# Performance work log

Measured on AMD Instinct MI355X. Metric: run time of the kernel, lower is better.

## Reference

```python
import jax, jax.numpy as jnp
import numpy as np

B, N, D = 64, 128, 32
P = N * (N - 1)          # ordered pairs
H1, H2, HF = 32, 32, 16  # layer_widths=(32,32), final_widths=(16,)
EPS = 1e-5
SLOPE = 0.01             # LeakyReLU default


def _leaky(x):
    return jnp.where(x >= 0, x, SLOPE * x)


def setup_inputs() -> dict:
    key = jax.random.key(0)
    ks = jax.random.split(key, 16)
    # all ordered pairs (i, j), i != j, grouped by source i
    src = np.repeat(np.arange(N), N - 1)
    tgt = np.array([j for i in range(N) for j in range(N) if j != i])
    s = 0.1
    return {
        "inputs": jax.random.normal(ks[0], (B, N, D), jnp.float32),
        "src": jnp.asarray(src, jnp.int32),
        "tgt": jnp.asarray(tgt, jnp.int32),
        # edge MLP: Linear(2D,32) -> BN1d(P) -> LeakyReLU -> Linear(32,32) -> LeakyReLU -> Linear(32, 1+D)
        "W1": jax.random.normal(ks[1], (2 * D, H1), jnp.float32) * s,
        "b1": jnp.zeros((H1,), jnp.float32),
        "g1": jnp.ones((P,), jnp.float32),
        "be1": jnp.zeros((P,), jnp.float32),
        "W2": jax.random.normal(ks[2], (H1, H2), jnp.float32) * s,
        "b2": jnp.zeros((H2,), jnp.float32),
        "W3": jax.random.normal(ks[3], (H2, 1 + D), jnp.float32) * s,
        "b3": jnp.zeros((1 + D,), jnp.float32),
        # final MLP: Linear(2D,16) -> BN1d(16) -> LeakyReLU -> Linear(16, D)
        "Wf1": jax.random.normal(ks[4], (2 * D, HF), jnp.float32) * s,
        "bf1": jnp.zeros((HF,), jnp.float32),
        "gf": jnp.ones((HF,), jnp.float32),
        "bef": jnp.zeros((HF,), jnp.float32),
        "Wf2": jax.random.normal(ks[5], (HF, D), jnp.float32) * s,
        "bf2": jnp.zeros((D,), jnp.float32),
    }


def reference(inputs, src, tgt, W1, b1, g1, be1, W2, b2, W3, b3,
              Wf1, bf1, gf, bef, Wf2, bf2):
    b, n, d = inputs.shape
    # gather pair features: (B, P, 2D)
    paired = jnp.concatenate([inputs[:, src], inputs[:, tgt]], axis=2)
    h = paired @ W1 + b1                              # (B, P, H1)
    # BatchNorm1d(P) on (B, P, H1): normalize per pair channel over (batch, feat)
    m = h.mean(axis=(0, 2), keepdims=True)
    v = h.var(axis=(0, 2), keepdims=True)
    h = (h - m) * jax.lax.rsqrt(v + EPS) * g1[None, :, None] + be1[None, :, None]
    h = _leaky(h) @ W2 + b2
    h = _leaky(h) @ W3 + b3                           # (B, P, 1+D)
    edges = jax.nn.sigmoid(h[..., :1])                # (B, P, 1)
    messages = h[..., 1:]                             # (B, P, D)
    weighted = edges * messages
    # segment-sum over the (N-1) senders per source node
    agg = weighted.reshape(b, n, n - 1, d).sum(axis=2)  # (B, N, D)
    sm = jnp.concatenate([inputs, agg], axis=2).reshape(-1, 2 * d)
    f = sm @ Wf1 + bf1                                # (B*N, HF)
    mf = f.mean(axis=0)
    vf = f.var(axis=0)
    f = (f - mf) * jax.lax.rsqrt(vf + EPS) * gf + bef
    out = _leaky(f) @ Wf2 + bf2
    return edges[..., 0], out.reshape(b, n, d)
```

## Files before the change

### kernel.cpp

```cpp
#include <hip/hip_runtime.h>
#include <hip/hip_bf16.h>
#include <math.h>

#define BB 64
#define NN 128
#define DD 32
#define PP (NN * (NN - 1))
#define EPSF 1e-5f

typedef __attribute__((ext_vector_type(8))) short bf16x8;
typedef __attribute__((ext_vector_type(4))) float f32x4;

static __device__ __forceinline__ unsigned short f2bf(float x) {
    unsigned u = __builtin_bit_cast(unsigned, x);
    u += 0x7fff + ((u >> 16) & 1);
    return (unsigned short)(u >> 16);
}
static __device__ __forceinline__ unsigned pk2bf(float a, float b) {
    float2 t; t.x = a; t.y = b;
    __hip_bfloat162 h = __float22bfloat162_rn(t);
    unsigned u;
    __builtin_memcpy(&u, &h, 4);
    return u;
}
static __device__ __forceinline__ float leakyf(float x) {
    return fmaxf(x, 0.01f * x);
}

__global__ __launch_bounds__(256) void proj_kernel(
    const float* __restrict__ inputs, const float* __restrict__ W1,
    const float* __restrict__ b1,
    const float* __restrict__ W2, const float* __restrict__ W3,
    float* __restrict__ AT, float* __restrict__ BT,
    unsigned short* __restrict__ ATh, unsigned short* __restrict__ BTh,
    float* __restrict__ SQp,
    unsigned short* __restrict__ W2p, unsigned short* __restrict__ W3p,
    float* __restrict__ fpartA, float* __restrict__ fpartB)
{
    __shared__ float Xs[16 * 33];
    __shared__ float W1s[2048];
    __shared__ float red[16];

    int tid = threadIdx.x;
    int n = blockIdx.x >> 2, q = blockIdx.x & 3;

    for (int idx = tid; idx < 2048; idx += 256) W1s[idx] = W1[idx];
    for (int idx = tid; idx < 512; idx += 256) {
        int r = idx >> 5, d = idx & 31;
        Xs[r * 33 + d] = inputs[(size_t)(q * 16 + r) * 4096 + n * 32 + d];
    }
    __syncthreads();

    int j = tid & 31, rb = tid >> 5;
    int lane = tid & 63, w = tid >> 6;
    float b1j = b1[j];
    float sa = 0.f, qa = 0.f, sb = 0.f, qb = 0.f;
    #pragma unroll
    for (int i = 0; i < 2; ++i) {
        int r = rb * 2 + i;
        int b = q * 16 + r;
        float a = b1j, c = 0.f;
        #pragma unroll
        for (int k = 0; k < 32; ++k) {
            float x = Xs[r * 33 + k];
            a += x * W1s[k * 32 + j];
            c += x * W1s[(32 + k) * 32 + j];
        }
        size_t off = ((size_t)n * 64 + b) * 32 + j;
        AT[off] = a;  BT[off] = c;
        ATh[off] = f2bf(a);  BTh[off] = f2bf(c);
        sa += a; qa += a * a; sb += c; qb += c * c;
    }
    #pragma unroll
    for (int d = 32; d > 0; d >>= 1) {
        sa += __shfl_down(sa, d, 64);
        qa += __shfl_down(qa, d, 64);
        sb += __shfl_down(sb, d, 64);
        qb += __shfl_down(qb, d, 64);
    }
    if (lane == 0) { red[w*4+0] = sa; red[w*4+1] = qa; red[w*4+2] = sb; red[w*4+3] = qb; }
    __syncthreads();
    if (tid == 0) {
        float4 v;
        v.x = red[0] + red[4] + red[8]  + red[12];
        v.y = red[1] + red[5] + red[9]  + red[13];
        v.z = red[2] + red[6] + red[10] + red[14];
        v.w = red[3] + red[7] + red[11] + red[15];
        ((float4*)SQp)[n * 4 + q] = v;
    }

    if (blockIdx.x == 0 && tid < 64) {
        int l = tid, nn2 = l & 15, kc = l >> 4;
        #pragma unroll
        for (int ct = 0; ct < 2; ++ct)
            #pragma unroll
            for (int jj = 0; jj < 8; ++jj) {
                int k = kc * 8 + jj;
                W2p[(ct * 64 + l) * 8 + jj] = f2bf(W2[k * 32 + ct * 16 + nn2]);
            }
        #pragma unroll
        for (int ct = 0; ct < 3; ++ct)
            #pragma unroll
            for (int jj = 0; jj < 8; ++jj) {
                int k = kc * 8 + jj;
                int c2 = ct * 16 + nn2;
                W3p[(ct * 64 + l) * 8 + jj] = f2bf(c2 < 33 ? W3[k * 33 + c2] : 0.f);
            }
    }
    if (blockIdx.x == 1) {
        for (int idx = tid; idx < 1024; idx += 256) {
            fpartA[idx] = 0.f;
            fpartB[idx] = 0.f;
        }
    }
}

__global__ __launch_bounds__(256) void stats2_kernel(
    const unsigned short* __restrict__ ATh, const unsigned short* __restrict__ BTh,
    const float* __restrict__ SQp,
    const float* __restrict__ g1, const float* __restrict__ be1,
    float* __restrict__ statA, float* __restrict__ statB)
{
    __shared__ __align__(16) float part[4 * 64 * 4];
    int tid = threadIdx.x;
    int lane = tid & 63, w = tid >> 6;
    int s0 = (blockIdx.x >> 3) * 16, t0 = (blockIdx.x & 7) * 16;

    int m = lane & 15, kc = lane >> 4;
    const unsigned short* abase = ATh + (size_t)(s0 + m) * 2048 + kc * 8 + w * 512;
    const unsigned short* bbase = BTh + (size_t)(t0 + m) * 2048 + kc * 8 + w * 512;

    f32x4 acc0 = {0.f, 0.f, 0.f, 0.f}, acc1 = {0.f, 0.f, 0.f, 0.f};
    #pragma unroll
    for (int step = 0; step < 8; ++step) {
        bf16x8 av0 = *(const bf16x8*)(abase + (2 * step) * 32);
        bf16x8 bv0 = *(const bf16x8*)(bbase + (2 * step) * 32);
        acc0 = __builtin_amdgcn_mfma_f32_16x16x32_bf16(av0, bv0, acc0, 0, 0, 0);
        bf16x8 av1 = *(const bf16x8*)(abase + (2 * step + 1) * 32);
        bf16x8 bv1 = *(const bf16x8*)(bbase + (2 * step + 1) * 32);
        acc1 = __builtin_amdgcn_mfma_f32_16x16x32_bf16(av1, bv1, acc1, 0, 0, 0);
    }
    f32x4 acc;
    acc[0] = acc0[0] + acc1[0]; acc[1] = acc0[1] + acc1[1];
    acc[2] = acc0[2] + acc1[2]; acc[3] = acc0[3] + acc1[3];
    *(f32x4*)&part[(w * 64 + lane) * 4] = acc;
    __syncthreads();

    if (w == 0) {
        #pragma unroll
        for (int ww = 1; ww < 4; ++ww) {
            f32x4 o2 = *(const f32x4*)&part[(ww * 64 + lane) * 4];
            acc[0] += o2[0]; acc[1] += o2[1]; acc[2] += o2[2]; acc[3] += o2[3];
        }
        int col = lane & 15, quad = lane >> 4;
        int t = t0 + col;
        float sbt = 0.f, qbt = 0.f;
        #pragma unroll
        for (int o2 = 0; o2 < 4; ++o2) {
            float4 v = ((const float4*)SQp)[t * 4 + o2];
            sbt += v.z; qbt += v.w;
        }
        #pragma unroll
        for (int r = 0; r < 4; ++r) {
            int s = s0 + quad * 4 + r;
            if (s != t) {
                float sas = 0.f, qas = 0.f;
                #pragma unroll
                for (int o2 = 0; o2 < 4; ++o2) {
                    float4 v = ((const float4*)SQp)[s * 4 + o2];
                    sas += v.x; qas += v.y;
                }
                int e = t - (t > s);
                int p = s * 127 + e;
                float S = sas + sbt;
                float Q = qas + qbt + 2.f * acc[r];
                float mean = S * (1.f / 2048.f);
                float var  = Q * (1.f / 2048.f) - mean * mean;
                float inv  = rsqrtf(var + EPSF);
                float sc   = inv * g1[p];
                statA[p] = sc;
                statB[p] = be1[p] - mean * sc;
            }
        }
    }
}

__global__ __launch_bounds__(256) void edges_kernel(
    const float* __restrict__ AT, const float* __restrict__ BT,
    const float* __restrict__ statA, const float* __restrict__ statB,
    const unsigned short* __restrict__ W2p, const unsigned short* __restrict__ W3p,
    const float* __restrict__ b2, const float* __restrict__ b3,
    const float* __restrict__ inputs, const float* __restrict__ Wf1,
    const float* __restrict__ bf1,
    float* __restrict__ edges_out,
    float* __restrict__ f, float* __restrict__ fpartA, float* __restrict__ fpartB)
{
    __shared__ __align__(16) unsigned short Hs[4][512];
    __shared__ float Wf1s[1024];
    __shared__ float aggbuf[4][32];

    int tid = threadIdx.x;
    int s = blockIdx.x & 127;
    int b = blockIdx.x >> 7;
    int lane = tid & 63, w = tid >> 6;
    int m = lane & 15;
    int kb = lane >> 4;
    int col = m;
    int q4 = kb * 4;
    int qbase = lane & 48;

    for (int idx = tid; idx < 1024; idx += 256) Wf1s[idx] = Wf1[idx];

    bf16x8 wb2[2], wb3[3];
    wb2[0] = *(const bf16x8*)(W2p + (0 * 64 + lane) * 8);
    wb2[1] = *(const bf16x8*)(W2p + (1 * 64 + lane) * 8);
    wb3[0] = *(const bf16x8*)(W3p + (0 * 64 + lane) * 8);
    wb3[1] = *(const bf16x8*)(W3p + (1 * 64 + lane) * 8);
    wb3[2] = *(const bf16x8*)(W3p + (2 * 64 + lane) * 8);
    float b2c0 = b2[col], b2c1 = b2[16 + col];
    float b3c[3];
    #pragma unroll
    for (int ct = 0; ct < 3; ++ct) {
        int c = ct * 16 + col;
        b3c[ct] = (c < 33) ? b3[c] : 0.f;
    }

    const float4* asl = (const float4*)(AT + ((size_t)s * 64 + b) * 32 + kb * 8);
    float4 a0 = asl[0], a1 = asl[1];

    float aggpart[3] = {0.f, 0.f, 0.f};

    #pragma unroll
    for (int rt = 0; rt < 2; ++rt) {
        int tile = w * 2 + rt;
        int e = tile * 16 + m;
        bool valid = (e < 127);
        int ee = valid ? e : 0;
        int t = ee + (ee >= s);
        int p = s * 127 + ee;
        float sc = statA[p], sh = statB[p];

        const float4* bsl = (const float4*)(BT + ((size_t)t * 64 + b) * 32 + kb * 8);
        float4 bv0 = bsl[0], bv1 = bsl[1];

        float nh[8];
        nh[0] = leakyf((a0.x + bv0.x) * sc + sh);
        nh[1] = leakyf((a0.y + bv0.y) * sc + sh);
        nh[2] = leakyf((a0.z + bv0.z) * sc + sh);
        nh[3] = leakyf((a0.w + bv0.w) * sc + sh);
        nh[4] = leakyf((a1.x + bv1.x) * sc + sh);
        nh[5] = leakyf((a1.y + bv1.y) * sc + sh);
        nh[6] = leakyf((a1.z + bv1.z) * sc + sh);
        nh[7] = leakyf((a1.w + bv1.w) * sc + sh);
        if (!valid) {
            #pragma unroll
            for (int q = 0; q < 8; ++q) nh[q] = 0.f;
        }
        union { bf16x8 v; unsigned u[4]; } AF;
        #pragma unroll
        for (int q = 0; q < 4; ++q) AF.u[q] = pk2bf(nh[2*q], nh[2*q+1]);

        f32x4 c0 = {0.f, 0.f, 0.f, 0.f}, c1 = {0.f, 0.f, 0.f, 0.f};
        c0 = __builtin_amdgcn_mfma_f32_16x16x32_bf16(AF.v, wb2[0], c0, 0, 0, 0);
        c1 = __builtin_amdgcn_mfma_f32_16x16x32_bf16(AF.v, wb2[1], c1, 0, 0, 0);

        #pragma unroll
        for (int reg = 0; reg < 4; ++reg) {
            int row = q4 + reg;
            float x = leakyf(c0[reg] + b2c0);
            float y = leakyf(c1[reg] + b2c1);
            int cA = col;
            int cB = col + 16;
            Hs[w][row * 32 + (((cA >> 3) ^ (row >> 2)) & 3) * 8 + (cA & 7)] = f2bf(x);
            Hs[w][row * 32 + (((cB >> 3) ^ (row >> 2)) & 3) * 8 + (cB & 7)] = f2bf(y);
        }
        bf16x8 a2 = *(const bf16x8*)&Hs[w][m * 32 + ((kb ^ (m >> 2)) & 3) * 8];

        f32x4 oo[3];
        #pragma unroll
        for (int ct = 0; ct < 3; ++ct) {
            f32x4 cc = {0.f, 0.f, 0.f, 0.f};
            oo[ct] = __builtin_amdgcn_mfma_f32_16x16x32_bf16(a2, wb3[ct], cc, 0, 0, 0);
        }

        float v0 = 0.f, v1 = 0.f, v2 = 0.f, v3 = 0.f;
        int grow0 = tile * 16 + q4;
        if (col == 0) {
            v0 = 1.f / (1.f + __expf(-(oo[0][0] + b3c[0])));
            v1 = 1.f / (1.f + __expf(-(oo[0][1] + b3c[0])));
            v2 = 1.f / (1.f + __expf(-(oo[0][2] + b3c[0])));
            v3 = (grow0 == 124) ? 0.f
               : 1.f / (1.f + __expf(-(oo[0][3] + b3c[0])));
            float* ep = edges_out + (size_t)b * PP + s * 127 + grow0;
            ep[0] = v0; ep[1] = v1; ep[2] = v2;
            if (grow0 != 124) ep[3] = v3;
        }
        float ev0 = __shfl(v0, qbase, 64);
        float ev1 = __shfl(v1, qbase, 64);
        float ev2 = __shfl(v2, qbase, 64);
        float ev3 = __shfl(v3, qbase, 64);

        #pragma unroll
        for (int ct = 0; ct < 3; ++ct) {
            float bb3 = b3c[ct];
            float pt = ev0 * (oo[ct][0] + bb3) + ev1 * (oo[ct][1] + bb3)
                     + ev2 * (oo[ct][2] + bb3) + ev3 * (oo[ct][3] + bb3);
            aggpart[ct] += pt;
        }
    }

    #pragma unroll
    for (int ct = 0; ct < 3; ++ct) {
        float pt = aggpart[ct];
        pt += __shfl_xor(pt, 16, 64);
        pt += __shfl_xor(pt, 32, 64);
        int c = ct * 16 + col;
        if (kb == 0 && c >= 1 && c <= 32) aggbuf[w][c - 1] = pt;
    }
    __syncthreads();

    if (tid < 16) {
        size_t row = (size_t)b * 128 + s;
        const float* xrow = inputs + row * 32;
        float acc = bf1[tid];
        #pragma unroll
        for (int k = 0; k < 32; ++k) acc += xrow[k] * Wf1s[k * 16 + tid];
        #pragma unroll
        for (int k = 0; k < 32; ++k) {
            float tot = aggbuf[0][k] + aggbuf[1][k] + aggbuf[2][k] + aggbuf[3][k];
            acc += tot * Wf1s[(32 + k) * 16 + tid];
        }
        f[row * 16 + tid] = acc;
        int bucket = blockIdx.x & 63;
        atomicAdd(&fpartA[bucket * 16 + tid], acc);
        atomicAdd(&fpartB[bucket * 16 + tid], acc * acc);
    }
}

__global__ __launch_bounds__(256) void out_kernel(
    const float* __restrict__ f,
    const float* __restrict__ fpartA, const float* __restrict__ fpartB,
    const float* __restrict__ gf, const float* __restrict__ bef,
    const float* __restrict__ Wf2, const float* __restrict__ bf2,
    float* __restrict__ outp)
{
    __shared__ float Wf2s[512];
    __shared__ float sc[16], sh[16];
    __shared__ float fs[128];

    int tid = threadIdx.x;
    for (int idx = tid; idx < 512; idx += 256) Wf2s[idx] = Wf2[idx];
    if (tid < 16) {
        float S = 0.f, Q = 0.f;
        #pragma unroll
        for (int g = 0; g < 64; ++g) {
            S += fpartA[g * 16 + tid];
            Q += fpartB[g * 16 + tid];
        }
        float mean = S * (1.f / 8192.f);
        float var  = Q * (1.f / 8192.f) - mean * mean;
        float inv  = rsqrtf(var + EPSF);
        float s2   = inv * gf[tid];
        sc[tid] = s2;
        sh[tid] = bef[tid] - mean * s2;
    }
    int row0 = blockIdx.x * 8;
    if (tid < 128) {
        int r = tid >> 4, j = tid & 15;
        fs[r * 16 + j] = f[(size_t)(row0 + r) * 16 + j];
    }
    __syncthreads();

    int rl = tid >> 5, d = tid & 31;
    float acc = bf2[d];
    #pragma unroll
    for (int j = 0; j < 16; ++j) {
        float v = fs[rl * 16 + j] * sc[j] + sh[j];
        v = leakyf(v);
        acc += v * Wf2s[j * 32 + d];
    }
    outp[(size_t)(row0 + rl) * 32 + d] = acc;
}

extern "C" void kernel_launch(void* const* d_in, const int* in_sizes, int n_in,
                              void* d_out, int out_size, void* d_ws, size_t ws_size,
                              hipStream_t stream) {
    const float* inputs = (const float*)d_in[0];
    const float* W1   = (const float*)d_in[3];
    const float* b1   = (const float*)d_in[4];
    const float* g1   = (const float*)d_in[5];
    const float* be1  = (const float*)d_in[6];
    const float* W2   = (const float*)d_in[7];
    const float* b2   = (const float*)d_in[8];
    const float* W3   = (const float*)d_in[9];
    const float* b3   = (const float*)d_in[10];
    const float* Wf1  = (const float*)d_in[11];
    const float* bf1  = (const float*)d_in[12];
    const float* gf   = (const float*)d_in[13];
    const float* bef  = (const float*)d_in[14];
    const float* Wf2  = (const float*)d_in[15];
    const float* bf2  = (const float*)d_in[16];

    float* ws = (float*)d_ws;
    float* AT     = ws;
    float* BT     = ws + 262144;
    unsigned short* ATh = (unsigned short*)(ws + 524288);
    unsigned short* BTh = ATh + 262144;
    float* SQp    = ws + 786432;
    float* statA  = ws + 790528;
    float* statB  = ws + 806784;
    float* f      = ws + 823040;
    float* fpartA = ws + 954112;
    float* fpartB = ws + 955136;
    unsigned short* W2p = (unsigned short*)(ws + 956160);
    unsigned short* W3p = W2p + 1024;

    float* edges_out = (float*)d_out;
    float* outp      = edges_out + (size_t)BB * PP;

    proj_kernel<<<512, 256, 0, stream>>>(inputs, W1, b1, W2, W3,
                                         AT, BT, ATh, BTh, SQp,
                                         W2p, W3p, fpartA, fpartB);
    stats2_kernel<<<64, 256, 0, stream>>>(ATh, BTh, SQp, g1, be1, statA, statB);
    edges_kernel<<<8192, 256, 0, stream>>>(AT, BT, statA, statB, W2p, W3p,
                                           b2, b3, inputs, Wf1, bf1,
                                           edges_out, f, fpartA, fpartB);
    out_kernel<<<1024, 256, 0, stream>>>(f, fpartA, fpartB, gf, bef, Wf2, bf2, outp);
}
```

Baseline: 144.2 us.

## Micro-optimize edges kernel: packed stats, packed-float math, 32-bit indexing, parallel Wf1 tail

```diff
diff --git a/kernel.cpp b/kernel.cpp
--- a/kernel.cpp
+++ b/kernel.cpp
@@ -10,18 +10,17 @@
 
 typedef __attribute__((ext_vector_type(8))) short bf16x8;
 typedef __attribute__((ext_vector_type(4))) float f32x4;
-
-static __device__ __forceinline__ unsigned short f2bf(float x) {
-    unsigned u = __builtin_bit_cast(unsigned, x);
-    u += 0x7fff + ((u >> 16) & 1);
-    return (unsigned short)(u >> 16);
-}
+typedef __attribute__((ext_vector_type(2))) float f32x2;
+
 static __device__ __forceinline__ unsigned pk2bf(float a, float b) {
     float2 t; t.x = a; t.y = b;
     __hip_bfloat162 h = __float22bfloat162_rn(t);
     unsigned u;
     __builtin_memcpy(&u, &h, 4);
     return u;
+}
+static __device__ __forceinline__ unsigned short f2bf(float x) {
+    return (unsigned short)pk2bf(x, x);
 }
 static __device__ __forceinline__ float leakyf(float x) {
     return fmaxf(x, 0.01f * x);
@@ -47,7 +46,7 @@
     for (int idx = tid; idx < 2048; idx += 256) W1s[idx] = W1[idx];
     for (int idx = tid; idx < 512; idx += 256) {
         int r = idx >> 5, d = idx & 31;
-        Xs[r * 33 + d] = inputs[(size_t)(q * 16 + r) * 4096 + n * 32 + d];
+        Xs[r * 33 + d] = inputs[(q * 16 + r) * 4096 + n * 32 + d];
     }
     __syncthreads();
 
@@ -66,7 +65,7 @@
             a += x * W1s[k * 32 + j];
             c += x * W1s[(32 + k) * 32 + j];
         }
-        size_t off = ((size_t)n * 64 + b) * 32 + j;
+        int off = (n * 64 + b) * 32 + j;
         AT[off] = a;  BT[off] = c;
         ATh[off] = f2bf(a);  BTh[off] = f2bf(c);
         sa += a; qa += a * a; sb += c; qb += c * c;
@@ -119,7 +118,7 @@
     const unsigned short* __restrict__ ATh, const unsigned short* __restrict__ BTh,
     const float* __restrict__ SQp,
     const float* __restrict__ g1, const float* __restrict__ be1,
-    float* __restrict__ statA, float* __restrict__ statB)
+    float* __restrict__ statAB)
 {
     __shared__ __align__(16) float part[4 * 64 * 4];
     int tid = threadIdx.x;
@@ -127,8 +126,8 @@
     int s0 = (blockIdx.x >> 3) * 16, t0 = (blockIdx.x & 7) * 16;
 
     int m = lane & 15, kc = lane >> 4;
-    const unsigned short* abase = ATh + (size_t)(s0 + m) * 2048 + kc * 8 + w * 512;
-    const unsigned short* bbase = BTh + (size_t)(t0 + m) * 2048 + kc * 8 + w * 512;
+    const unsigned short* abase = ATh + (s0 + m) * 2048 + kc * 8 + w * 512;
+    const unsigned short* bbase = BTh + (t0 + m) * 2048 + kc * 8 + w * 512;
 
     f32x4 acc0 = {0.f, 0.f, 0.f, 0.f}, acc1 = {0.f, 0.f, 0.f, 0.f};
     #pragma unroll
@@ -178,16 +177,18 @@
                 float var  = Q * (1.f / 2048.f) - mean * mean;
                 float inv  = rsqrtf(var + EPSF);
                 float sc   = inv * g1[p];
-                statA[p] = sc;
-                statB[p] = be1[p] - mean * sc;
+                float2 o;
+                o.x = sc;
+                o.y = be1[p] - mean * sc;
+                ((float2*)statAB)[p] = o;
             }
         }
     }
 }
 
-__global__ __launch_bounds__(256) void edges_kernel(
+__global__ __launch_bounds__(256, 8) void edges_kernel(
     const float* __restrict__ AT, const float* __restrict__ BT,
-    const float* __restrict__ statA, const float* __restrict__ statB,
+    const float* __restrict__ statAB,
     const unsigned short* __restrict__ W2p, const unsigned short* __restrict__ W3p,
     const float* __restrict__ b2, const float* __restrict__ b3,
     const float* __restrict__ inputs, const float* __restrict__ Wf1,
@@ -225,8 +226,11 @@
         b3c[ct] = (c < 33) ? b3[c] : 0.f;
     }
 
-    const float4* asl = (const float4*)(AT + ((size_t)s * 64 + b) * 32 + kb * 8);
+    const float4* asl = (const float4*)(AT + (s * 64 + b) * 32 + kb * 8);
     float4 a0 = asl[0], a1 = asl[1];
+    f32x2 av[4];
+    av[0][0]=a0.x; av[0][1]=a0.y; av[1][0]=a0.z; av[1][1]=a0.w;
+    av[2][0]=a1.x; av[2][1]=a1.y; av[3][0]=a1.z; av[3][1]=a1.w;
 
     float aggpart[3] = {0.f, 0.f, 0.f};
 
@@ -238,27 +242,27 @@
         int ee = valid ? e : 0;
         int t = ee + (ee >= s);
         int p = s * 127 + ee;
-        float sc = statA[p], sh = statB[p];
-
-        const float4* bsl = (const float4*)(BT + ((size_t)t * 64 + b) * 32 + kb * 8);
+        float2 st = ((const float2*)statAB)[p];
+        float sc = valid ? st.x : 0.f;
+        float sh = valid ? st.y : 0.f;
+        f32x2 sc2; sc2[0] = sc; sc2[1] = sc;
+        f32x2 sh2; sh2[0] = sh; sh2[1] = sh;
+
+        const float4* bsl = (const float4*)(BT + (t * 64 + b) * 32 + kb * 8);
         float4 bv0 = bsl[0], bv1 = bsl[1];
-
-        float nh[8];
-        nh[0] = leakyf((a0.x + bv0.x) * sc + sh);
-        nh[1] = leakyf((a0.y + bv0.y) * sc + sh);
-        nh[2] = leakyf((a0.z + bv0.z) * sc + sh);
-        nh[3] = leakyf((a0.w + bv0.w) * sc + sh);
-        nh[4] = leakyf((a1.x + bv1.x) * sc + sh);
-        nh[5] = leakyf((a1.y + bv1.y) * sc + sh);
-        nh[6] = leakyf((a1.z + bv1.z) * sc + sh);
-        nh[7] = leakyf((a1.w + bv1.w) * sc + sh);
-        if (!valid) {
-            #pragma unroll
-            for (int q = 0; q < 8; ++q) nh[q] = 0.f;
-        }
+        f32x2 bv[4];
+        bv[0][0]=bv0.x; bv[0][1]=bv0.y; bv[1][0]=bv0.z; bv[1][1]=bv0.w;
+        bv[2][0]=bv1.x; bv[2][1]=bv1.y; bv[3][0]=bv1.z; bv[3][1]=bv1.w;
+
         union { bf16x8 v; unsigned u[4]; } AF;
         #pragma unroll
-        for (int q = 0; q < 4; ++q) AF.u[q] = pk2bf(nh[2*q], nh[2*q+1]);
+        for (int i = 0; i < 4; ++i) {
+            f32x2 y = (av[i] + bv[i]) * sc2 + sh2;
+            f32x2 tq = y * 0.01f;
+            float n0 = fmaxf(y[0], tq[0]);
+            float n1 = fmaxf(y[1], tq[1]);
+            AF.u[i] = pk2bf(n0, n1);
+        }
 
         f32x4 c0 = {0.f, 0.f, 0.f, 0.f}, c1 = {0.f, 0.f, 0.f, 0.f};
         c0 = __builtin_amdgcn_mfma_f32_16x16x32_bf16(AF.v, wb2[0], c0, 0, 0, 0);
@@ -291,7 +295,7 @@
             v2 = 1.f / (1.f + __expf(-(oo[0][2] + b3c[0])));
             v3 = (grow0 == 124) ? 0.f
                : 1.f / (1.f + __expf(-(oo[0][3] + b3c[0])));
-            float* ep = edges_out + (size_t)b * PP + s * 127 + grow0;
+            float* ep = edges_out + b * PP + s * 127 + grow0;
             ep[0] = v0; ep[1] = v1; ep[2] = v2;
             if (grow0 != 124) ep[3] = v3;
         }
@@ -319,21 +323,34 @@
     }
     __syncthreads();
 
-    if (tid < 16) {
-        size_t row = (size_t)b * 128 + s;
+    if (w == 0) {
+        int j = lane & 15, kg = lane >> 4;
+        int row = b * 128 + s;
         const float* xrow = inputs + row * 32;
-        float acc = bf1[tid];
-        #pragma unroll
-        for (int k = 0; k < 32; ++k) acc += xrow[k] * Wf1s[k * 16 + tid];
-        #pragma unroll
-        for (int k = 0; k < 32; ++k) {
-            float tot = aggbuf[0][k] + aggbuf[1][k] + aggbuf[2][k] + aggbuf[3][k];
-            acc += tot * Wf1s[(32 + k) * 16 + tid];
-        }
-        f[row * 16 + tid] = acc;
-        int bucket = blockIdx.x & 63;
-        atomicAdd(&fpartA[bucket * 16 + tid], acc);
-        atomicAdd(&fpartB[bucket * 16 + tid], acc * acc);
+        float acc = 0.f;
+        if (kg < 2) {
+            #pragma unroll
+            for (int i = 0; i < 16; ++i) {
+                int k = kg * 16 + i;
+                acc += xrow[k] * Wf1s[k * 16 + j];
+            }
+        } else {
+            #pragma unroll
+            for (int i = 0; i < 16; ++i) {
+                int k = (kg - 2) * 16 + i;
+                float tot = aggbuf[0][k] + aggbuf[1][k] + aggbuf[2][k] + aggbuf[3][k];
+                acc += tot * Wf1s[(32 + k) * 16 + j];
+            }
+        }
+        acc += __shfl_xor(acc, 16, 64);
+        acc += __shfl_xor(acc, 32, 64);
+        if (lane < 16) {
+            acc += bf1[j];
+            f[row * 16 + j] = acc;
+            int bucket = blockIdx.x & 63;
+            atomicAdd(&fpartA[bucket * 16 + j], acc);
+            atomicAdd(&fpartB[bucket * 16 + j], acc * acc);
+        }
     }
 }
 
@@ -367,7 +384,7 @@
     int row0 = blockIdx.x * 8;
     if (tid < 128) {
         int r = tid >> 4, j = tid & 15;
-        fs[r * 16 + j] = f[(size_t)(row0 + r) * 16 + j];
+        fs[r * 16 + j] = f[(row0 + r) * 16 + j];
     }
     __syncthreads();
 
@@ -379,7 +396,7 @@
         v = leakyf(v);
         acc += v * Wf2s[j * 32 + d];
     }
-    outp[(size_t)(row0 + rl) * 32 + d] = acc;
+    outp[(row0 + rl) * 32 + d] = acc;
 }
 
 extern "C" void kernel_launch(void* const* d_in, const int* in_sizes, int n_in,
@@ -407,8 +424,7 @@
     unsigned short* ATh = (unsigned short*)(ws + 524288);
     unsigned short* BTh = ATh + 262144;
     float* SQp    = ws + 786432;
-    float* statA  = ws + 790528;
-    float* statB  = ws + 806784;
+    float* statAB = ws + 790528;
     float* f      = ws + 823040;
     float* fpartA = ws + 954112;
     float* fpartB = ws + 955136;
@@ -421,8 +437,8 @@
     proj_kernel<<<512, 256, 0, stream>>>(inputs, W1, b1, W2, W3,
                                          AT, BT, ATh, BTh, SQp,
                                          W2p, W3p, fpartA, fpartB);
-    stats2_kernel<<<64, 256, 0, stream>>>(ATh, BTh, SQp, g1, be1, statA, statB);
-    edges_kernel<<<8192, 256, 0, stream>>>(AT, BT, statA, statB, W2p, W3p,
+    stats2_kernel<<<64, 256, 0, stream>>>(ATh, BTh, SQp, g1, be1, statAB);
+    edges_kernel<<<8192, 256, 0, stream>>>(AT, BT, statAB, W2p, W3p,
                                            b2, b3, inputs, Wf1, bf1,
                                            edges_out, f, fpartA, fpartB);
     out_kernel<<<1024, 256, 0, stream>>>(f, fpartA, fpartB, gf, bef, Wf2, bf2, outp);
```

Measured after the change: 146.2 us. Within noise of the previous version (+1.4%).
